# Optimization experiments

Measured on AMD Instinct MI355X. Metric: run time of the kernel, lower is better.

## Reference

```python
import jax, jax.numpy as jnp
import numpy as np

N = 10000
E = 256000
MUL = 32            # multiplicity per l (hidden_sizes = [32]*4)
NB = 10             # nbasis_funcs
RMAX = 3.5          # max_radius
NAVG = 25.6         # navg_neighbors
NGRAPH = 16         # number of graphs in batch
SLICES = [(0, 1), (1, 4), (4, 9), (9, 16)]  # l=0..3 blocks of the 16-dim SH rep


def _sph_harm(u):
    """Real spherical harmonics l=0..3, component normalization, on unit vectors. [E,16]"""
    x, y, z = u[:, 0], u[:, 1], u[:, 2]
    one = jnp.ones_like(x)
    s3 = 3.0 ** 0.5
    s15 = 15.0 ** 0.5
    s5 = 5.0 ** 0.5
    a = (35.0 / 8.0) ** 0.5
    b = 105.0 ** 0.5
    c = (21.0 / 8.0) ** 0.5
    d = 7.0 ** 0.5 / 2.0
    cols = [
        one,
        s3 * x, s3 * y, s3 * z,
        s15 * x * y, s15 * y * z, 0.5 * s5 * (3 * z * z - 1), s15 * x * z, 0.5 * s15 * (x * x - y * y),
        a * y * (3 * x * x - y * y), b * x * y * z, c * y * (5 * z * z - 1), d * z * (5 * z * z - 3),
        c * x * (5 * z * z - 1), 0.5 * b * z * (x * x - y * y), a * x * (x * x - 3 * y * y),
    ]
    return jnp.stack(cols, axis=1)


def _radial(emb, W1, W2):
    # FullyConnectedNet-style MLP with fan-in normalization and silu
    h = jax.nn.silu(emb @ W1 / (NB ** 0.5))
    return h @ W2 / (W1.shape[1] ** 0.5)


def _edge_geometry(pos, edge_src, edge_dst):
    vec = pos[edge_src] - pos[edge_dst]          # [E,3]
    r = jnp.linalg.norm(vec, axis=1)             # [E]
    u = vec / (r[:, None] + 1e-9)
    sh = _sph_harm(u)                            # [E,16]
    t = jnp.clip(r / RMAX, 0.0, 1.0)
    cutoff = jnp.where(r < RMAX, 0.5 * (jnp.cos(jnp.pi * t) + 1.0), 0.0)
    edge_attr = cutoff[:, None] * sh             # [E,16]
    centers = jnp.linspace(0.0, RMAX, NB)
    step = RMAX / (NB - 1)
    emb = jnp.exp(-(((r[:, None] - centers) / step) ** 2)) / 1.12 * (NB ** 0.5)
    return edge_attr, emb


def _layer(feat, edge_src, edge_dst, edge_attr, emb, Wsc, Wr1, Wr2):
    """Gated interaction block: self-connection + per-edge radial-weighted TP conv + gate."""
    n = feat.shape[0]
    # self-connection: per-l channel mixing
    sc = jnp.concatenate(
        [jnp.einsum('nci,co->noi', feat[:, :, a:b], Wsc[l]) for l, (a, b) in enumerate(SLICES)],
        axis=2) / (MUL ** 0.5)
    # per-edge weights from radial MLP: [E, 2 paths, 4 l's, MUL]
    w = _radial(emb, Wr1, Wr2).reshape(-1, 2, 4, MUL)
    xs = feat[edge_src]                          # [E,MUL,16] gather
    # path A (0e x Yl -> l) for l=0, plus path B (l x Yl -> 0e) for l=1..3 -> scalar slot
    scal = w[:, 0, 0, :] * xs[:, :, 0] * edge_attr[:, 0:1]
    parts = []
    for l, (a, b) in enumerate(SLICES):
        if l == 0:
            continue
        scal = scal + w[:, 1, l, :] * jnp.einsum('eci,ei->ec', xs[:, :, a:b], edge_attr[:, a:b])
        parts.append(w[:, 0, l, :, None] * xs[:, :, 0:1] * edge_attr[:, None, a:b])
    msg = jnp.concatenate([scal[:, :, None]] + parts, axis=2)   # [E,MUL,16]
    agg = jax.ops.segment_sum(msg, edge_dst, num_segments=n) / (NAVG ** 0.5)
    y = sc + agg
    # equivariant gate: silu on scalars, sigmoid(scalar) gates l>0 features
    s = y[:, :, 0]
    return jnp.concatenate(
        [jax.nn.silu(s)[:, :, None], y[:, :, 1:] * jax.nn.sigmoid(s)[:, :, None]], axis=2)


def _forward(pos, x, batch, edge_src, edge_dst, W_sc, Wr1, Wr2, Wf1, Wf2):
    n = pos.shape[0]
    edge_attr, emb = _edge_geometry(pos, edge_src, edge_dst)
    # lift scalar input features into the full l=0..3 layout
    feat = jnp.zeros((n, MUL, 16), x.dtype).at[:, :, 0].set(x)
    for i in range(3):
        feat = _layer(feat, edge_src, edge_dst, edge_attr, emb, W_sc[i], Wr1[i], Wr2[i])
    # final interaction block -> 1x0e output per node
    wf = _radial(emb, Wf1, Wf2).reshape(-1, 4, MUL)             # [E,4,MUL]
    xs = feat[edge_src]
    ms = wf[:, 0, :] * xs[:, :, 0] * edge_attr[:, 0:1]
    for l, (a, b) in enumerate(SLICES):
        if l == 0:
            continue
        ms = ms + wf[:, l, :] * jnp.einsum('eci,ei->ec', xs[:, :, a:b], edge_attr[:, a:b])
    node = jax.ops.segment_sum(ms.sum(axis=1) / (MUL ** 0.5), edge_dst, num_segments=n) / (NAVG ** 0.5)
    out = jax.ops.segment_sum(node, batch, num_segments=NGRAPH) / (NAVG ** 0.5)
    return out.flatten()


def setup_inputs() -> dict:
    key = jax.random.key(0)
    ks = jax.random.split(key, 10)
    pos = jax.random.uniform(ks[0], (N, 3), jnp.float32) * 5.0
    x = jax.random.normal(ks[1], (N, MUL), jnp.float32)
    batch = jnp.sort(jax.random.randint(ks[2], (N,), 0, NGRAPH, jnp.int32))
    edge_src = jax.random.randint(ks[3], (E,), 0, N, jnp.int32)
    edge_dst = jax.random.randint(ks[4], (E,), 0, N, jnp.int32)
    W_sc = jax.random.normal(ks[5], (3, 4, MUL, MUL), jnp.float32)
    Wr1 = jax.random.normal(ks[6], (3, NB, 64), jnp.float32)
    Wr2 = jax.random.normal(ks[7], (3, 64, 2 * 4 * MUL), jnp.float32)
    Wf1 = jax.random.normal(ks[8], (NB, 64), jnp.float32)
    Wf2 = jax.random.normal(ks[9], (64, 4 * MUL), jnp.float32)
    return {"pos": pos, "x": x, "batch": batch, "edge_src": edge_src, "edge_dst": edge_dst,
            "W_sc": W_sc, "Wr1": Wr1, "Wr2": Wr2, "Wf1": Wf1, "Wf2": Wf2}


def reference(pos, x, batch, edge_src, edge_dst, W_sc, Wr1, Wr2, Wf1, Wf2):
    return _forward(pos, x, batch, edge_src, edge_dst, W_sc, Wr1, Wr2, Wf1, Wf2)
```

## Files before the change

### kernel.cpp

```cpp
#include <hip/hip_runtime.h>
#include <math.h>

#define NN 10000
#define EE 256000
#define NGR 16
#define ECAP 150016

#define RSQRT10F   0.31622776601683794f
#define EMB_SCALE  2.8234621965789103f
#define INV_SQRT_MUL  0.17677669529663687f
#define INV_SQRT_NAVG 0.19764235376052372f
#define SCREC      (0.125f * INV_SQRT_NAVG)
#define STEPF      0.3888888888888889f
#define INV_STEPF  2.5714285714285716f
#define PIF        3.14159265358979323846f

__device__ __forceinline__ float sigm(float x) {
    return 1.0f / (1.0f + __expf(-x));
}

__device__ __forceinline__ void atomAddF(float* p, float v) {
    __hip_atomic_fetch_add(p, v, __ATOMIC_RELAXED, __HIP_MEMORY_SCOPE_AGENT);
}

__global__ __launch_bounds__(256) void count_kernel(
    const float* __restrict__ pos, const int* __restrict__ esrc,
    const int* __restrict__ edst, int* __restrict__ deg)
{
    int e = blockIdx.x * 256 + threadIdx.x;
    if (e >= EE) return;
    int s = esrc[e], d = edst[e];
    float vx = pos[3*s+0] - pos[3*d+0];
    float vy = pos[3*s+1] - pos[3*d+1];
    float vz = pos[3*s+2] - pos[3*d+2];
    float r2 = vx*vx + vy*vy + vz*vz;
    if (r2 < 12.25f) atomicAdd(&deg[d], 1);
}

__global__ __launch_bounds__(256) void scan_kernel(
    const int* __restrict__ deg, int* __restrict__ off, int* __restrict__ cursor)
{
    __shared__ int sbuf[256];
    const int t = threadIdx.x;
    const int start = t * 40;
    const int end = (start + 40 < NN) ? start + 40 : NN;
    int s = 0;
    for (int i = start; i < end; ++i) s += deg[i];
    sbuf[t] = s;
    __syncthreads();
    for (int d = 1; d < 256; d <<= 1) {
        int v = (t >= d) ? sbuf[t - d] : 0;
        __syncthreads();
        sbuf[t] += v;
        __syncthreads();
    }
    int run = sbuf[t] - s;
    for (int i = start; i < end; ++i) {
        off[i] = run; cursor[i] = run; run += deg[i];
    }
    if (t == 255) off[NN] = sbuf[255];
}

__global__ __launch_bounds__(256) void w1t_kernel(
    const float* __restrict__ Wr1, const float* __restrict__ Wf1,
    float* __restrict__ w1t)
{
    int t = blockIdx.x * 256 + threadIdx.x;
    if (t >= 4096) return;
    int i = t & 15;
    int j = (t >> 4) & 63;
    int l = t >> 10;
    float v;
    if (l < 3) v = (i < 10) ? Wr1[l * 640 + i * 64 + j] : 0.0f;
    else       v = (i < 10) ? Wf1[i * 64 + j] : 0.0f;
    w1t[l * 1024 + j * 16 + i] = v;
}

__global__ __launch_bounds__(256) void pack_kernel(
    const float* __restrict__ Wr2, const float* __restrict__ Wf2,
    float* __restrict__ wr2p, float* __restrict__ wf2p)
{
    const int offs[7] = {0, 32, 64, 96, 160, 192, 224};
    int t = blockIdx.x * 256 + threadIdx.x;
    if (t < 49152) {
        int k = t & 63;
        int j = (t >> 6) & 63;
        int g = (t >> 12) & 3;
        int layer = t >> 14;
        float v = 0.0f;
        if (k < 56)
            v = Wr2[layer * 16384 + j * 256 + offs[k >> 3] + g * 8 + (k & 7)];
        wr2p[t] = v;
    } else if (t < 49152 + 8192) {
        int t2 = t - 49152;
        int k = t2 & 31;
        int j = (t2 >> 5) & 63;
        int g = t2 >> 11;
        wf2p[t2] = Wf2[j * 128 + (k >> 3) * 32 + g * 8 + (k & 7)];
    }
}

__global__ __launch_bounds__(256) void scatter_kernel(
    const float* __restrict__ pos, const int* __restrict__ esrc,
    const int* __restrict__ edst, int* __restrict__ cursor,
    int* __restrict__ csrc, int* __restrict__ cdst,
    float* __restrict__ attr_soa, float* __restrict__ attr_e,
    float* __restrict__ emb_soa)
{
    int e = blockIdx.x * 256 + threadIdx.x;
    if (e >= EE) return;
    int s = esrc[e], d = edst[e];
    float vx = pos[3*s+0] - pos[3*d+0];
    float vy = pos[3*s+1] - pos[3*d+1];
    float vz = pos[3*s+2] - pos[3*d+2];
    float r2 = vx*vx + vy*vy + vz*vz;
    if (r2 >= 12.25f) return;
    float r = sqrtf(r2);
    int slot = atomicAdd(&cursor[d], 1);
    if (slot >= ECAP) return;

    float inv = 1.0f / (r + 1e-9f);
    float x = vx * inv, y = vy * inv, z = vz * inv;

    float t = r * (1.0f / 3.5f);
    float cw = 0.5f * (cosf(PIF * t) + 1.0f);

    const float s3  = 1.7320508075688772f;
    const float s15 = 3.872983346207417f;
    const float s5  = 2.23606797749979f;
    const float a4  = 2.0916500663351889f;
    const float b4  = 10.246950765959598f;
    const float c4  = 1.6201851746019651f;
    const float d4  = 1.3228756555322954f;
    float xx = x*x, yy = y*y, zz = z*z;
    float sh[16];
    sh[0]  = 1.0f;
    sh[1]  = s3 * x;
    sh[2]  = s3 * y;
    sh[3]  = s3 * z;
    sh[4]  = s15 * x * y;
    sh[5]  = s15 * y * z;
    sh[6]  = 0.5f * s5 * (3.0f*zz - 1.0f);
    sh[7]  = s15 * x * z;
    sh[8]  = 0.5f * s15 * (xx - yy);
    sh[9]  = a4 * y * (3.0f*xx - yy);
    sh[10] = b4 * x * y * z;
    sh[11] = c4 * y * (5.0f*zz - 1.0f);
    sh[12] = d4 * z * (5.0f*zz - 3.0f);
    sh[13] = c4 * x * (5.0f*zz - 1.0f);
    sh[14] = 0.5f * b4 * z * (xx - yy);
    sh[15] = a4 * x * (xx - 3.0f*yy);

    float4* ae = (float4*)(attr_e + (size_t)slot * 16);
    #pragma unroll
    for (int q = 0; q < 4; ++q)
        ae[q] = make_float4(cw*sh[q*4], cw*sh[q*4+1], cw*sh[q*4+2], cw*sh[q*4+3]);

    #pragma unroll
    for (int i = 0; i < 16; ++i)
        attr_soa[(size_t)i * ECAP + slot] = cw * sh[i];
    #pragma unroll
    for (int k = 0; k < 10; ++k) {
        float dd = (r - (float)k * STEPF) * INV_STEPF;
        emb_soa[(size_t)k * ECAP + slot] = __expf(-dd * dd) * EMB_SCALE;
    }
    csrc[slot] = s;
    cdst[slot] = d;
}

__global__ __launch_bounds__(256) void init_feat_kernel(
    const float* __restrict__ x, float* __restrict__ feat)
{
    int t = blockIdx.x * 256 + threadIdx.x;
    if (t >= NN * 512) return;
    int i = t & 15;
    int c = (t >> 4) & 31;
    int n = t >> 9;
    feat[t] = (i == 0) ? x[n * 32 + c] : 0.0f;
}

__global__ __launch_bounds__(256) void h_kernel(
    const float* __restrict__ w1t, const float* __restrict__ emb_soa,
    float* __restrict__ h_soa, const int* __restrict__ cntp)
{
    const int tid = threadIdx.x;
    int cnt = *cntp; if (cnt > ECAP) cnt = ECAP;
    if (cnt == 0) return;
    const int e = blockIdx.x * 256 + tid;
    if (blockIdx.x * 256 >= cnt) return;
    const bool alive = (e < cnt);
    const int ee = alive ? e : (cnt - 1);

    float emb[10];
    #pragma unroll
    for (int i = 0; i < 10; ++i)
        emb[i] = emb_soa[(size_t)i * ECAP + ee];

    #pragma unroll 4
    for (int j = 0; j < 64; ++j) {
        const float* wj = w1t + j * 16;
        float a = 0.0f;
        #pragma unroll
        for (int i = 0; i < 10; ++i)
            a += emb[i] * wj[i];
        a *= RSQRT10F;
        if (alive)
            h_soa[(size_t)j * ECAP + e] = a * sigm(a);
    }
}

__global__ __launch_bounds__(256, 4) void edge_mlp_kernel(
    const float* __restrict__ wr2p, const float* __restrict__ h_soa,
    const float* __restrict__ fin, float* __restrict__ rec,
    const int* __restrict__ csrc,
    const float* __restrict__ attr_soa, const int* __restrict__ cntp)
{
    const int tid = threadIdx.x;
    const int g = blockIdx.x;
    const int c0 = g * 8;
    int cnt = *cntp; if (cnt > ECAP) cnt = ECAP;
    if (cnt == 0) return;
    const int e = blockIdx.y * 256 + tid;
    if (blockIdx.y * 256 >= cnt) return;
    const bool alive = (e < cnt);
    const int ee = alive ? e : (cnt - 1);

    float attr[16];
    #pragma unroll
    for (int i = 0; i < 16; ++i)
        attr[i] = attr_soa[(size_t)i * ECAP + ee];

    const float* xb = fin + (size_t)csrc[ee] * 512;
    const float* hp = h_soa + ee;
    const float* wg = wr2p + (size_t)g * 4096;
    float4* rec4 = (float4*)rec;

    float a0[8], a1[8], a2[8], a3[8], a4[8], a5[8], a6[8];
    #pragma unroll
    for (int u = 0; u < 8; ++u) {
        a0[u] = 0.f; a1[u] = 0.f; a2[u] = 0.f; a3[u] = 0.f;
        a4[u] = 0.f; a5[u] = 0.f; a6[u] = 0.f;
    }
    #pragma unroll 8
    for (int j = 0; j < 64; ++j) {
        const float hj = hp[(size_t)j * ECAP];
        const float* w = wg + j * 64;
        #pragma unroll
        for (int u = 0; u < 8; ++u) {
            a0[u] += hj * w[u];
            a1[u] += hj * w[8 + u];
            a2[u] += hj * w[16 + u];
            a3[u] += hj * w[24 + u];
            a4[u] += hj * w[32 + u];
            a5[u] += hj * w[40 + u];
            a6[u] += hj * w[48 + u];
        }
    }
    #pragma unroll
    for (int u = 0; u < 8; ++u) {
        const int c = c0 + u;
        const float4* xv = (const float4*)(xb + c * 16);
        float4 x0 = xv[0], x1 = xv[1], x2 = xv[2], x3 = xv[3];
        float d1 = x0.y*attr[1] + x0.z*attr[2] + x0.w*attr[3];
        float d2 = x1.x*attr[4] + x1.y*attr[5] + x1.z*attr[6]
                 + x1.w*attr[7] + x2.x*attr[8];
        float d3 = x2.y*attr[9] + x2.z*attr[10] + x2.w*attr[11]
                 + x3.x*attr[12] + x3.y*attr[13] + x3.z*attr[14]
                 + x3.w*attr[15];
        const float xs0 = x0.x;
        float scal = SCREC * (a0[u]*xs0*attr[0] + a4[u]*d1 + a5[u]*d2 + a6[u]*d3);
        float px = SCREC * xs0;
        if (alive)
            rec4[(size_t)c * ECAP + e] =
                make_float4(scal, a1[u] * px, a2[u] * px, a3[u] * px);
    }
}

__global__ __launch_bounds__(256) void agg_kernel(
    const float* __restrict__ fin, float* __restrict__ fout,
    const float* __restrict__ Wsc, const float* __restrict__ rec,
    const float* __restrict__ attr_e, const int* __restrict__ off)
{
    int t = blockIdx.x * 256 + threadIdx.x;
    int c = t & 31;
    int n = t >> 5;
    if (n >= NN) return;

    float acc[16];
    #pragma unroll
    for (int i = 0; i < 16; ++i) acc[i] = 0.0f;

    const float* f = fin + (size_t)n * 512;
    for (int cin = 0; cin < 32; ++cin) {
        float w0 = Wsc[          cin * 32 + c];
        float w1 = Wsc[1024 + cin * 32 + c];
        float w2 = Wsc[2048 + cin * 32 + c];
        float w3 = Wsc[3072 + cin * 32 + c];
        const float4* fv = (const float4*)(f + cin * 16);
        float4 f0 = fv[0], f1 = fv[1], f2 = fv[2], f3 = fv[3];
        acc[0]  += f0.x * w0;
        acc[1]  += f0.y * w1; acc[2]  += f0.z * w1; acc[3]  += f0.w * w1;
        acc[4]  += f1.x * w2; acc[5]  += f1.y * w2; acc[6]  += f1.z * w2;
        acc[7]  += f1.w * w2; acc[8]  += f2.x * w2;
        acc[9]  += f2.y * w3; acc[10] += f2.z * w3; acc[11] += f2.w * w3;
        acc[12] += f3.x * w3; acc[13] += f3.y * w3; acc[14] += f3.z * w3;
        acc[15] += f3.w * w3;
    }
    #pragma unroll
    for (int i = 0; i < 16; ++i) acc[i] *= INV_SQRT_MUL;

    const float4* rec4 = (const float4*)rec;
    int e0 = off[n], e1 = off[n + 1];
    if (e1 > ECAP) e1 = ECAP;
    for (int e = e0; e < e1; ++e) {
        float4 v = rec4[(size_t)c * ECAP + e];
        const float4* av = (const float4*)(attr_e + (size_t)e * 16);
        float4 A0 = av[0], A1 = av[1], A2 = av[2], A3 = av[3];
        acc[0]  += v.x;
        acc[1]  += v.y * A0.y;
        acc[2]  += v.y * A0.z;
        acc[3]  += v.y * A0.w;
        acc[4]  += v.z * A1.x;
        acc[5]  += v.z * A1.y;
        acc[6]  += v.z * A1.z;
        acc[7]  += v.z * A1.w;
        acc[8]  += v.z * A2.x;
        acc[9]  += v.w * A2.y;
        acc[10] += v.w * A2.z;
        acc[11] += v.w * A2.w;
        acc[12] += v.w * A3.x;
        acc[13] += v.w * A3.y;
        acc[14] += v.w * A3.z;
        acc[15] += v.w * A3.w;
    }

    float s = acc[0];
    float g = sigm(s);
    float4 o0 = make_float4(s * g,      acc[1] * g,  acc[2] * g,  acc[3] * g);
    float4 o1 = make_float4(acc[4] * g, acc[5] * g,  acc[6] * g,  acc[7] * g);
    float4 o2 = make_float4(acc[8] * g, acc[9] * g,  acc[10] * g, acc[11] * g);
    float4 o3 = make_float4(acc[12] * g, acc[13] * g, acc[14] * g, acc[15] * g);
    float4* ov = (float4*)(fout + (size_t)n * 512 + c * 16);
    ov[0] = o0; ov[1] = o1; ov[2] = o2; ov[3] = o3;
}

__global__ __launch_bounds__(256, 4) void final_edge_kernel(
    const float* __restrict__ wf2p, const float* __restrict__ h_soa,
    const float* __restrict__ fin, float* __restrict__ node,
    const int* __restrict__ csrc, const int* __restrict__ cdst,
    const float* __restrict__ attr_soa, const int* __restrict__ cntp)
{
    const int tid = threadIdx.x;
    const int g = blockIdx.x;
    const int c0 = g * 8;
    int cnt = *cntp; if (cnt > ECAP) cnt = ECAP;
    if (cnt == 0) return;
    const int e = blockIdx.y * 256 + tid;
    if (blockIdx.y * 256 >= cnt) return;
    const bool alive = (e < cnt);
    const int ee = alive ? e : (cnt - 1);

    float attr[16];
    #pragma unroll
    for (int i = 0; i < 16; ++i)
        attr[i] = attr_soa[(size_t)i * ECAP + ee];

    const float* xb = fin + (size_t)csrc[ee] * 512;
    const float* hp = h_soa + ee;
    const float* wg = wf2p + (size_t)g * 2048;

    float a0[8], a1[8], a2[8], a3[8];
    #pragma unroll
    for (int u = 0; u < 8; ++u) { a0[u]=0.f; a1[u]=0.f; a2[u]=0.f; a3[u]=0.f; }
    #pragma unroll 8
    for (int j = 0; j < 64; ++j) {
        const float hj = hp[(size_t)j * ECAP];
        const float* w = wg + j * 32;
        #pragma unroll
        for (int u = 0; u < 8; ++u) {
            a0[u] += hj * w[u];
            a1[u] += hj * w[8 + u];
            a2[u] += hj * w[16 + u];
            a3[u] += hj * w[24 + u];
        }
    }
    float msum = 0.0f;
    #pragma unroll
    for (int u = 0; u < 8; ++u) {
        const int c = c0 + u;
        const float4* xv = (const float4*)(xb + c * 16);
        float4 x0 = xv[0], x1 = xv[1], x2 = xv[2], x3 = xv[3];
        float d1 = x0.y*attr[1] + x0.z*attr[2] + x0.w*attr[3];
        float d2 = x1.x*attr[4] + x1.y*attr[5] + x1.z*attr[6]
                 + x1.w*attr[7] + x2.x*attr[8];
        float d3 = x2.y*attr[9] + x2.z*attr[10] + x2.w*attr[11]
                 + x3.x*attr[12] + x3.y*attr[13] + x3.z*attr[14]
                 + x3.w*attr[15];
        msum += 0.125f * (a0[u]*x0.x*attr[0] + a1[u]*d1 + a2[u]*d2 + a3[u]*d3);
    }
    if (alive)
        atomAddF(node + cdst[ee], msum * (INV_SQRT_MUL * INV_SQRT_NAVG));
}

__global__ __launch_bounds__(256) void out_kernel(
    const float* __restrict__ node, const int* __restrict__ batch,
    float* __restrict__ out)
{
    __shared__ float bins[NGR];
    int t = blockIdx.x * 256 + threadIdx.x;
    if (threadIdx.x < NGR) bins[threadIdx.x] = 0.0f;
    __syncthreads();
    if (t < NN) atomicAdd(&bins[batch[t]], node[t] * INV_SQRT_NAVG);
    __syncthreads();
    if (threadIdx.x < NGR) atomAddF(out + threadIdx.x, bins[threadIdx.x]);
}

extern "C" void kernel_launch(void* const* d_in, const int* in_sizes, int n_in,
                              void* d_out, int out_size, void* d_ws, size_t ws_size,
                              hipStream_t stream)
{
    const float* pos  = (const float*)d_in[0];
    const float* x    = (const float*)d_in[1];
    const int*   batch= (const int*)  d_in[2];
    const int*   esrc = (const int*)  d_in[3];
    const int*   edst = (const int*)  d_in[4];
    const float* W_sc = (const float*)d_in[5];
    const float* Wr1  = (const float*)d_in[6];
    const float* Wr2  = (const float*)d_in[7];
    const float* Wf1  = (const float*)d_in[8];
    const float* Wf2  = (const float*)d_in[9];
    float* out = (float*)d_out;

    char* ws = (char*)d_ws;
    size_t off_b = 0;
    auto alloc = [&](size_t bytes) -> void* {
        void* p = ws + off_b;
        off_b = (off_b + bytes + 255) & ~(size_t)255;
        return p;
    };
    int*   deg      = (int*)  alloc((size_t)NN * 4);
    int*   off      = (int*)  alloc((size_t)(NN + 1) * 4);
    int*   cursor   = (int*)  alloc((size_t)NN * 4);
    float* node     = (float*)alloc((size_t)NN * 4);
    int*   csrc     = (int*)  alloc((size_t)ECAP * 4);
    int*   cdst     = (int*)  alloc((size_t)ECAP * 4);
    float* w1t      = (float*)alloc((size_t)4 * 1024 * 4);
    float* wr2p     = (float*)alloc((size_t)3 * 16384 * 4);
    float* wf2p     = (float*)alloc((size_t)8192 * 4);
    float* emb_soa  = (float*)alloc((size_t)10 * ECAP * 4);
    float* attr_soa = (float*)alloc((size_t)16 * ECAP * 4);
    float* attr_e   = (float*)alloc((size_t)16 * ECAP * 4);
    float* h_soa    = (float*)alloc((size_t)64 * ECAP * 4);
    float* rec      = (float*)alloc((size_t)128 * ECAP * 4);
    float* feat_a   = (float*)alloc((size_t)NN * 512 * 4);
    float* feat_b   = (float*)alloc((size_t)NN * 512 * 4);

    hipMemsetAsync(deg, 0, (size_t)NN * 4, stream);
    hipMemsetAsync(node, 0, (size_t)NN * 4, stream);
    hipMemsetAsync(d_out, 0, (size_t)out_size * 4, stream);

    count_kernel<<<(EE + 255) / 256, 256, 0, stream>>>(pos, esrc, edst, deg);
    scan_kernel<<<1, 256, 0, stream>>>(deg, off, cursor);
    w1t_kernel<<<16, 256, 0, stream>>>(Wr1, Wf1, w1t);
    pack_kernel<<<(49152 + 8192 + 255) / 256, 256, 0, stream>>>(
        Wr2, Wf2, wr2p, wf2p);
    scatter_kernel<<<(EE + 255) / 256, 256, 0, stream>>>(
        pos, esrc, edst, cursor, csrc, cdst, attr_soa, attr_e, emb_soa);
    init_feat_kernel<<<(NN * 512 + 255) / 256, 256, 0, stream>>>(x, feat_a);

    const int* cntp = off + NN;
    float* fin = feat_a;
    float* fout = feat_b;
    dim3 egrid(4, ECAP / 256);
    for (int layer = 0; layer < 3; ++layer) {
        h_kernel<<<ECAP / 256, 256, 0, stream>>>(
            w1t + layer * 1024, emb_soa, h_soa, cntp);
        edge_mlp_kernel<<<egrid, 256, 0, stream>>>(
            wr2p + (size_t)layer * 16384, h_soa, fin, rec,
            csrc, attr_soa, cntp);
        agg_kernel<<<(NN * 32 + 255) / 256, 256, 0, stream>>>(
            fin, fout, W_sc + layer * 4096, rec, attr_e, off);
        float* tmp = fin; fin = fout; fout = tmp;
    }
    h_kernel<<<ECAP / 256, 256, 0, stream>>>(
        w1t + 3 * 1024, emb_soa, h_soa, cntp);
    final_edge_kernel<<<egrid, 256, 0, stream>>>(
        wf2p, h_soa, fin, node, csrc, cdst, attr_soa, cntp);
    out_kernel<<<(NN + 255) / 256, 256, 0, stream>>>(node, batch, out);
}
```

Measured before the change: 931.0 us.

## Restructure edge radial MLP as column-per-thread GEMM with LDS transpose

Edge weight kernels now assign one output weight column per thread over a tile of 16 (or 32) edges, reading hidden activations as broadcast float4 rows and transposing results through shared memory before the tensor-product epilogue. Weights are repacked into a jg-major float4 layout, and the redundant attr SoA buffer is dropped in favor of the AoS attr array. The final kernel reduces per-edge partials in LDS before one atomic per edge. This cuts the repeated reading of h across channel groups and lowers register pressure, but each block now rereads the full weight matrix and computes padded columns.

```diff
diff --git a/kernel.cpp b/kernel.cpp
--- a/kernel.cpp
+++ b/kernel.cpp
@@ -78,25 +78,28 @@
 
 __global__ __launch_bounds__(256) void pack_kernel(
     const float* __restrict__ Wr2, const float* __restrict__ Wf2,
-    float* __restrict__ wr2p, float* __restrict__ wf2p)
+    float* __restrict__ wr2q, float* __restrict__ wf2q)
 {
     const int offs[7] = {0, 32, 64, 96, 160, 192, 224};
     int t = blockIdx.x * 256 + threadIdx.x;
     if (t < 49152) {
-        int k = t & 63;
-        int j = (t >> 6) & 63;
-        int g = (t >> 12) & 3;
         int layer = t >> 14;
-        float v = 0.0f;
-        if (k < 56)
-            v = Wr2[layer * 16384 + j * 256 + offs[k >> 3] + g * 8 + (k & 7)];
-        wr2p[t] = v;
+        int r = t & 16383;
+        int jg = r >> 10;
+        int k = (r >> 2) & 255;
+        int jj = r & 3;
+        int j = jg * 4 + jj;
+        int slot = k >> 5, c = k & 31;
+        float v = (slot < 7)
+            ? Wr2[layer * 16384 + j * 256 + offs[slot] + c] : 0.0f;
+        wr2q[t] = v;
     } else if (t < 49152 + 8192) {
         int t2 = t - 49152;
-        int k = t2 & 31;
-        int j = (t2 >> 5) & 63;
-        int g = t2 >> 11;
-        wf2p[t2] = Wf2[j * 128 + (k >> 3) * 32 + g * 8 + (k & 7)];
+        int jg = t2 >> 9;
+        int k = (t2 >> 2) & 127;
+        int jj = t2 & 3;
+        int j = jg * 4 + jj;
+        wf2q[t2] = Wf2[j * 128 + k];
     }
 }
 
@@ -104,8 +107,7 @@
     const float* __restrict__ pos, const int* __restrict__ esrc,
     const int* __restrict__ edst, int* __restrict__ cursor,
     int* __restrict__ csrc, int* __restrict__ cdst,
-    float* __restrict__ attr_soa, float* __restrict__ attr_e,
-    float* __restrict__ emb_soa)
+    float* __restrict__ attr_e, float* __restrict__ emb_soa)
 {
     int e = blockIdx.x * 256 + threadIdx.x;
     if (e >= EE) return;
@@ -157,9 +159,6 @@
         ae[q] = make_float4(cw*sh[q*4], cw*sh[q*4+1], cw*sh[q*4+2], cw*sh[q*4+3]);
 
     #pragma unroll
-    for (int i = 0; i < 16; ++i)
-        attr_soa[(size_t)i * ECAP + slot] = cw * sh[i];
-    #pragma unroll
     for (int k = 0; k < 10; ++k) {
         float dd = (r - (float)k * STEPF) * INV_STEPF;
         emb_soa[(size_t)k * ECAP + slot] = __expf(-dd * dd) * EMB_SCALE;
@@ -209,70 +208,80 @@
     }
 }
 
-__global__ __launch_bounds__(256, 4) void edge_mlp_kernel(
-    const float* __restrict__ wr2p, const float* __restrict__ h_soa,
+__global__ __launch_bounds__(256, 4) void edge_gemm_kernel(
+    const float* __restrict__ wr2q, const float* __restrict__ h_soa,
     const float* __restrict__ fin, float* __restrict__ rec,
-    const int* __restrict__ csrc,
-    const float* __restrict__ attr_soa, const int* __restrict__ cntp)
-{
+    const int* __restrict__ csrc, const float* __restrict__ attr_e,
+    const int* __restrict__ cntp)
+{
+    __shared__ float ldsW[256 * 17];
     const int tid = threadIdx.x;
-    const int g = blockIdx.x;
-    const int c0 = g * 8;
     int cnt = *cntp; if (cnt > ECAP) cnt = ECAP;
     if (cnt == 0) return;
-    const int e = blockIdx.y * 256 + tid;
-    if (blockIdx.y * 256 >= cnt) return;
-    const bool alive = (e < cnt);
-    const int ee = alive ? e : (cnt - 1);
-
-    float attr[16];
+    const int e0 = blockIdx.x * 16;
+    if (e0 >= cnt) return;
+
+    float acc[16];
+    #pragma unroll
+    for (int i = 0; i < 16; ++i) acc[i] = 0.0f;
+
+    const float4* wq4 = (const float4*)wr2q;
+    #pragma unroll 2
+    for (int jg = 0; jg < 16; ++jg) {
+        float4 wq = wq4[jg * 256 + tid];
+        #pragma unroll
+        for (int jj = 0; jj < 4; ++jj) {
+            const float4* hr =
+                (const float4*)(h_soa + (size_t)(jg * 4 + jj) * ECAP + e0);
+            float4 h0 = hr[0], h1 = hr[1], h2 = hr[2], h3 = hr[3];
+            float w = (jj == 0) ? wq.x : (jj == 1) ? wq.y
+                    : (jj == 2) ? wq.z : wq.w;
+            acc[0]  += h0.x * w; acc[1]  += h0.y * w;
+            acc[2]  += h0.z * w; acc[3]  += h0.w * w;
+            acc[4]  += h1.x * w; acc[5]  += h1.y * w;
+            acc[6]  += h1.z * w; acc[7]  += h1.w * w;
+            acc[8]  += h2.x * w; acc[9]  += h2.y * w;
+            acc[10] += h2.z * w; acc[11] += h2.w * w;
+            acc[12] += h3.x * w; acc[13] += h3.y * w;
+            acc[14] += h3.z * w; acc[15] += h3.w * w;
+        }
+    }
     #pragma unroll
     for (int i = 0; i < 16; ++i)
-        attr[i] = attr_soa[(size_t)i * ECAP + ee];
-
-    const float* xb = fin + (size_t)csrc[ee] * 512;
-    const float* hp = h_soa + ee;
-    const float* wg = wr2p + (size_t)g * 4096;
+        ldsW[tid * 17 + i] = acc[i];
+    __syncthreads();
+
+    const int e = tid & 15;
+    const int ge = e0 + e;
+    const bool alive = (ge < cnt);
+    const int eidx = alive ? ge : (cnt - 1);
+    const float* xb = fin + (size_t)csrc[eidx] * 512;
+    const float4* av = (const float4*)(attr_e + (size_t)eidx * 16);
+    float4 A0 = av[0], A1 = av[1], A2 = av[2], A3 = av[3];
     float4* rec4 = (float4*)rec;
 
-    float a0[8], a1[8], a2[8], a3[8], a4[8], a5[8], a6[8];
-    #pragma unroll
-    for (int u = 0; u < 8; ++u) {
-        a0[u] = 0.f; a1[u] = 0.f; a2[u] = 0.f; a3[u] = 0.f;
-        a4[u] = 0.f; a5[u] = 0.f; a6[u] = 0.f;
-    }
-    #pragma unroll 8
-    for (int j = 0; j < 64; ++j) {
-        const float hj = hp[(size_t)j * ECAP];
-        const float* w = wg + j * 64;
-        #pragma unroll
-        for (int u = 0; u < 8; ++u) {
-            a0[u] += hj * w[u];
-            a1[u] += hj * w[8 + u];
-            a2[u] += hj * w[16 + u];
-            a3[u] += hj * w[24 + u];
-            a4[u] += hj * w[32 + u];
-            a5[u] += hj * w[40 + u];
-            a6[u] += hj * w[48 + u];
-        }
-    }
-    #pragma unroll
-    for (int u = 0; u < 8; ++u) {
-        const int c = c0 + u;
+    #pragma unroll
+    for (int pass = 0; pass < 2; ++pass) {
+        const int c = (tid >> 4) + pass * 16;
+        float w00 = ldsW[(0*32 + c) * 17 + e];
+        float w01 = ldsW[(1*32 + c) * 17 + e];
+        float w02 = ldsW[(2*32 + c) * 17 + e];
+        float w03 = ldsW[(3*32 + c) * 17 + e];
+        float w11 = ldsW[(4*32 + c) * 17 + e];
+        float w12 = ldsW[(5*32 + c) * 17 + e];
+        float w13 = ldsW[(6*32 + c) * 17 + e];
         const float4* xv = (const float4*)(xb + c * 16);
         float4 x0 = xv[0], x1 = xv[1], x2 = xv[2], x3 = xv[3];
-        float d1 = x0.y*attr[1] + x0.z*attr[2] + x0.w*attr[3];
-        float d2 = x1.x*attr[4] + x1.y*attr[5] + x1.z*attr[6]
-                 + x1.w*attr[7] + x2.x*attr[8];
-        float d3 = x2.y*attr[9] + x2.z*attr[10] + x2.w*attr[11]
-                 + x3.x*attr[12] + x3.y*attr[13] + x3.z*attr[14]
-                 + x3.w*attr[15];
-        const float xs0 = x0.x;
-        float scal = SCREC * (a0[u]*xs0*attr[0] + a4[u]*d1 + a5[u]*d2 + a6[u]*d3);
+        float d1 = x0.y*A0.y + x0.z*A0.z + x0.w*A0.w;
+        float d2 = x1.x*A1.x + x1.y*A1.y + x1.z*A1.z + x1.w*A1.w + x2.x*A2.x;
+        float d3 = x2.y*A2.y + x2.z*A2.z + x2.w*A2.w + x3.x*A3.x
+                 + x3.y*A3.y + x3.z*A3.z + x3.w*A3.w;
+        float xs0 = x0.x;
+        float scal = SCREC * (w00*xs0*A0.x + w11*d1 + w12*d2 + w13*d3);
         float px = SCREC * xs0;
         if (alive)
-            rec4[(size_t)c * ECAP + e] =
-                make_float4(scal, a1[u] * px, a2[u] * px, a3[u] * px);
+            rec4[(size_t)c * ECAP + ge] =
+                make_float4(scal, w01 * px, w02 * px, w03 * px);
     }
 }
 
@@ -344,62 +353,86 @@
     ov[0] = o0; ov[1] = o1; ov[2] = o2; ov[3] = o3;
 }
 
-__global__ __launch_bounds__(256, 4) void final_edge_kernel(
-    const float* __restrict__ wf2p, const float* __restrict__ h_soa,
+__global__ __launch_bounds__(256, 4) void final_gemm_kernel(
+    const float* __restrict__ wf2q, const float* __restrict__ h_soa,
     const float* __restrict__ fin, float* __restrict__ node,
     const int* __restrict__ csrc, const int* __restrict__ cdst,
-    const float* __restrict__ attr_soa, const int* __restrict__ cntp)
-{
+    const float* __restrict__ attr_e, const int* __restrict__ cntp)
+{
+    __shared__ float ldsW[128 * 33];
+    __shared__ float ldsR[32 * 8];
     const int tid = threadIdx.x;
-    const int g = blockIdx.x;
-    const int c0 = g * 8;
     int cnt = *cntp; if (cnt > ECAP) cnt = ECAP;
     if (cnt == 0) return;
-    const int e = blockIdx.y * 256 + tid;
-    if (blockIdx.y * 256 >= cnt) return;
-    const bool alive = (e < cnt);
-    const int ee = alive ? e : (cnt - 1);
-
-    float attr[16];
+    const int e0 = blockIdx.x * 32;
+    if (e0 >= cnt) return;
+    const int k = tid & 127;
+    const int half = tid >> 7;
+    const int eb = e0 + half * 16;
+
+    float acc[16];
+    #pragma unroll
+    for (int i = 0; i < 16; ++i) acc[i] = 0.0f;
+
+    const float4* wq4 = (const float4*)wf2q;
+    #pragma unroll 2
+    for (int jg = 0; jg < 16; ++jg) {
+        float4 wq = wq4[jg * 128 + k];
+        #pragma unroll
+        for (int jj = 0; jj < 4; ++jj) {
+            const float4* hr =
+                (const float4*)(h_soa + (size_t)(jg * 4 + jj) * ECAP + eb);
+            float4 h0 = hr[0], h1 = hr[1], h2 = hr[2], h3 = hr[3];
+            float w = (jj == 0) ? wq.x : (jj == 1) ? wq.y
+                    : (jj == 2) ? wq.z : wq.w;
+            acc[0]  += h0.x * w; acc[1]  += h0.y * w;
+            acc[2]  += h0.z * w; acc[3]  += h0.w * w;
+            acc[4]  += h1.x * w; acc[5]  += h1.y * w;
+            acc[6]  += h1.z * w; acc[7]  += h1.w * w;
+            acc[8]  += h2.x * w; acc[9]  += h2.y * w;
+            acc[10] += h2.z * w; acc[11] += h2.w * w;
+            acc[12] += h3.x * w; acc[13] += h3.y * w;
+            acc[14] += h3.z * w; acc[15] += h3.w * w;
+        }
+    }
     #pragma unroll
     for (int i = 0; i < 16; ++i)
-        attr[i] = attr_soa[(size_t)i * ECAP + ee];
-
-    const float* xb = fin + (size_t)csrc[ee] * 512;
-    const float* hp = h_soa + ee;
-    const float* wg = wf2p + (size_t)g * 2048;
-
-    float a0[8], a1[8], a2[8], a3[8];
-    #pragma unroll
-    for (int u = 0; u < 8; ++u) { a0[u]=0.f; a1[u]=0.f; a2[u]=0.f; a3[u]=0.f; }
-    #pragma unroll 8
-    for (int j = 0; j < 64; ++j) {
-        const float hj = hp[(size_t)j * ECAP];
-        const float* w = wg + j * 32;
-        #pragma unroll
-        for (int u = 0; u < 8; ++u) {
-            a0[u] += hj * w[u];
-            a1[u] += hj * w[8 + u];
-            a2[u] += hj * w[16 + u];
-            a3[u] += hj * w[24 + u];
-        }
-    }
-    float msum = 0.0f;
-    #pragma unroll
-    for (int u = 0; u < 8; ++u) {
-        const int c = c0 + u;
+        ldsW[k * 33 + half * 16 + i] = acc[i];
+    __syncthreads();
+
+    const int e = tid & 31;
+    const int cq = tid >> 5;
+    const int ge = e0 + e;
+    const bool alive = (ge < cnt);
+    const int eidx = alive ? ge : (cnt - 1);
+    const float* xb = fin + (size_t)csrc[eidx] * 512;
+    const float4* av = (const float4*)(attr_e + (size_t)eidx * 16);
+    float4 A0 = av[0], A1 = av[1], A2 = av[2], A3 = av[3];
+
+    float part = 0.0f;
+    #pragma unroll
+    for (int u = 0; u < 4; ++u) {
+        const int c = cq * 4 + u;
+        float a0 = ldsW[(0*32 + c) * 33 + e];
+        float a1 = ldsW[(1*32 + c) * 33 + e];
+        float a2 = ldsW[(2*32 + c) * 33 + e];
+        float a3 = ldsW[(3*32 + c) * 33 + e];
         const float4* xv = (const float4*)(xb + c * 16);
         float4 x0 = xv[0], x1 = xv[1], x2 = xv[2], x3 = xv[3];
-        float d1 = x0.y*attr[1] + x0.z*attr[2] + x0.w*attr[3];
-        float d2 = x1.x*attr[4] + x1.y*attr[5] + x1.z*attr[6]
-                 + x1.w*attr[7] + x2.x*attr[8];
-        float d3 = x2.y*attr[9] + x2.z*attr[10] + x2.w*attr[11]
-                 + x3.x*attr[12] + x3.y*attr[13] + x3.z*attr[14]
-                 + x3.w*attr[15];
-        msum += 0.125f * (a0[u]*x0.x*attr[0] + a1[u]*d1 + a2[u]*d2 + a3[u]*d3);
-    }
-    if (alive)
-        atomAddF(node + cdst[ee], msum * (INV_SQRT_MUL * INV_SQRT_NAVG));
+        float d1 = x0.y*A0.y + x0.z*A0.z + x0.w*A0.w;
+        float d2 = x1.x*A1.x + x1.y*A1.y + x1.z*A1.z + x1.w*A1.w + x2.x*A2.x;
+        float d3 = x2.y*A2.y + x2.z*A2.z + x2.w*A2.w + x3.x*A3.x
+                 + x3.y*A3.y + x3.z*A3.z + x3.w*A3.w;
+        part += 0.125f * (a0*x0.x*A0.x + a1*d1 + a2*d2 + a3*d3);
+    }
+    ldsR[e * 8 + cq] = part;
+    __syncthreads();
+    if (tid < 32 && (e0 + tid) < cnt) {
+        float s = 0.0f;
+        #pragma unroll
+        for (int q = 0; q < 8; ++q) s += ldsR[tid * 8 + q];
+        atomAddF(node + cdst[e0 + tid], s * (INV_SQRT_MUL * INV_SQRT_NAVG));
+    }
 }
 
 __global__ __launch_bounds__(256) void out_kernel(
@@ -445,10 +478,9 @@
     int*   csrc     = (int*)  alloc((size_t)ECAP * 4);
     int*   cdst     = (int*)  alloc((size_t)ECAP * 4);
     float* w1t      = (float*)alloc((size_t)4 * 1024 * 4);
-    float* wr2p     = (float*)alloc((size_t)3 * 16384 * 4);
-    float* wf2p     = (float*)alloc((size_t)8192 * 4);
+    float* wr2q     = (float*)alloc((size_t)3 * 16384 * 4);
+    float* wf2q     = (float*)alloc((size_t)8192 * 4);
     float* emb_soa  = (float*)alloc((size_t)10 * ECAP * 4);
-    float* attr_soa = (float*)alloc((size_t)16 * ECAP * 4);
     float* attr_e   = (float*)alloc((size_t)16 * ECAP * 4);
     float* h_soa    = (float*)alloc((size_t)64 * ECAP * 4);
     float* rec      = (float*)alloc((size_t)128 * ECAP * 4);
@@ -463,28 +495,27 @@
     scan_kernel<<<1, 256, 0, stream>>>(deg, off, cursor);
     w1t_kernel<<<16, 256, 0, stream>>>(Wr1, Wf1, w1t);
     pack_kernel<<<(49152 + 8192 + 255) / 256, 256, 0, stream>>>(
-        Wr2, Wf2, wr2p, wf2p);
+        Wr2, Wf2, wr2q, wf2q);
     scatter_kernel<<<(EE + 255) / 256, 256, 0, stream>>>(
-        pos, esrc, edst, cursor, csrc, cdst, attr_soa, attr_e, emb_soa);
+        pos, esrc, edst, cursor, csrc, cdst, attr_e, emb_soa);
     init_feat_kernel<<<(NN * 512 + 255) / 256, 256, 0, stream>>>(x, feat_a);
 
     const int* cntp = off + NN;
     float* fin = feat_a;
     float* fout = feat_b;
-    dim3 egrid(4, ECAP / 256);
     for (int layer = 0; layer < 3; ++layer) {
         h_kernel<<<ECAP / 256, 256, 0, stream>>>(
             w1t + layer * 1024, emb_soa, h_soa, cntp);
-        edge_mlp_kernel<<<egrid, 256, 0, stream>>>(
-            wr2p + (size_t)layer * 16384, h_soa, fin, rec,
-            csrc, attr_soa, cntp);
+        edge_gemm_kernel<<<ECAP / 16, 256, 0, stream>>>(
+            wr2q + (size_t)layer * 16384, h_soa, fin, rec,
+            csrc, attr_e, cntp);
         agg_kernel<<<(NN * 32 + 255) / 256, 256, 0, stream>>>(
             fin, fout, W_sc + layer * 4096, rec, attr_e, off);
         float* tmp = fin; fin = fout; fout = tmp;
     }
     h_kernel<<<ECAP / 256, 256, 0, stream>>>(
         w1t + 3 * 1024, emb_soa, h_soa, cntp);
-    final_edge_kernel<<<egrid, 256, 0, stream>>>(
-        wf2p, h_soa, fin, node, csrc, cdst, attr_soa, cntp);
+    final_gemm_kernel<<<ECAP / 32, 256, 0, stream>>>(
+        wf2q, h_soa, fin, node, csrc, cdst, attr_e, cntp);
     out_kernel<<<(NN + 255) / 256, 256, 0, stream>>>(node, batch, out);
 }
```

Result: slower. 955.3 us (+2.6%).
